# Performance work log

Hardware: AMD Instinct MI355X
Metric: run time of the kernel (lower is better)

Reference implementation:

```python
import jax, jax.numpy as jnp
import numpy as np

B = 16
NUM_CN = 25000
NUM_VN = 50000
NUM_EDGES = 200000
D_EMBED = 16
D_HIDDEN = 32
D_MSG = 16


def setup_inputs() -> dict:
    key = jax.random.key(0)
    ks = jax.random.split(key, 16)
    def w(k, fan_in, fan_out):
        return jax.random.normal(k, (fan_in, fan_out), dtype=jnp.float32) / jnp.sqrt(jnp.float32(fan_in))
    return {
        "h_from_x": jax.random.normal(ks[0], (B, NUM_CN, D_EMBED), dtype=jnp.float32),
        "h_from_z": jax.random.normal(ks[1], (B, NUM_CN, D_EMBED), dtype=jnp.float32),
        "h_to": jax.random.normal(ks[2], (B, NUM_VN, D_EMBED), dtype=jnp.float32),
        "syndrome_x": jax.random.randint(ks[3], (B, NUM_CN), 0, 2, dtype=jnp.int32),
        "syndrome_z": jax.random.randint(ks[4], (B, NUM_CN), 0, 2, dtype=jnp.int32),
        "from_ind_x": jax.random.randint(ks[5], (NUM_EDGES,), 0, NUM_CN, dtype=jnp.int32),
        "to_ind_x": jax.random.randint(ks[6], (NUM_EDGES,), 0, NUM_VN, dtype=jnp.int32),
        "from_ind_z": jax.random.randint(ks[7], (NUM_EDGES,), 0, NUM_CN, dtype=jnp.int32),
        "to_ind_z": jax.random.randint(ks[8], (NUM_EDGES,), 0, NUM_VN, dtype=jnp.int32),
        # msg MLP x: [2*D_EMBED -> D_HIDDEN (relu) -> D_MSG], no bias
        "Wx1": w(ks[9], 2 * D_EMBED, D_HIDDEN),
        "Wx2": w(ks[10], D_HIDDEN, D_MSG),
        "Wz1": w(ks[11], 2 * D_EMBED, D_HIDDEN),
        "Wz2": w(ks[12], D_HIDDEN, D_MSG),
        # embed MLP: [2*D_MSG + D_EMBED -> D_HIDDEN (relu) -> D_EMBED], no bias
        "We1": w(ks[13], 2 * D_MSG + D_EMBED, D_HIDDEN),
        "We2": w(ks[14], D_HIDDEN, D_EMBED),
    }


def _edge_messages(h_from, h_to, syn, from_ind, to_ind, W1, W2):
    # gather edge endpoint embeddings -> [B, E, 2*D_EMBED]
    feat = jnp.concatenate([h_from[:, from_ind, :], h_to[:, to_ind, :]], axis=-1)
    msg = jnp.maximum(feat @ W1, 0.0) @ W2          # [B, E, D_MSG]
    mask = syn[:, from_ind].astype(msg.dtype)[..., None]
    return msg * mask


def _segment_reduce_sum(msg, to_ind, num_vn):
    # ragged gather+sum per receiving vertex == segment_sum over to_ind
    # msg: [B, E, D] -> [E, B, D] -> segment_sum -> [N, B, D] -> [B, N, D]
    m = jax.ops.segment_sum(jnp.transpose(msg, (1, 0, 2)), to_ind, num_segments=num_vn)
    return jnp.transpose(m, (1, 0, 2))


def reference(h_from_x, h_from_z, h_to, syndrome_x, syndrome_z,
              from_ind_x, to_ind_x, from_ind_z, to_ind_z,
              Wx1, Wx2, Wz1, Wz2, We1, We2):
    num_vn = h_to.shape[1]
    msg_x = _edge_messages(h_from_x, h_to, syndrome_x, from_ind_x, to_ind_x, Wx1, Wx2)
    msg_z = _edge_messages(h_from_z, h_to, syndrome_z, from_ind_z, to_ind_z, Wz1, Wz2)
    m_x = _segment_reduce_sum(msg_x, to_ind_x, num_vn)  # [B, N, D_MSG]
    m_z = _segment_reduce_sum(msg_z, to_ind_z, num_vn)
    feat = jnp.concatenate([m_x, m_z, h_to], axis=-1)   # [B, N, 2*D_MSG+D_EMBED]
    h_to_new = jnp.maximum(feat @ We1, 0.0) @ We2
    return h_to_new
```

## Files before the change

kernel.cpp:

```cpp
#include <hip/hip_runtime.h>

#define NUM_CN   25000
#define NUM_VN   50000
#define NUM_E    200000
#define D_EMBED  16
#define D_HIDDEN 32
#define D_MSG    16
#define BATCH    16

#define WS_IDS_X   0
#define WS_IDS_Z   200000
#define WS_OFF_X   400000
#define WS_OFF_Z   450001
#define WS_CNT_X   500002
#define WS_CNT_Z   550002
#define WS_CUR_X   600002
#define WS_CUR_Z   650002
#define WS_INCL_X  700002
#define WS_INCL_Z  751202
#define WS_PSUM    802402
#define WS_BASE    802530
#define WS_A1X     802816
#define WS_A1Z     7202816
#define SCAN_CHUNKS 49

__global__ __launch_bounds__(256) void hist_kernel(
    const int* __restrict__ ti_x, const int* __restrict__ ti_z,
    int* __restrict__ cnt_x, int* __restrict__ cnt_z)
{
    int e = blockIdx.x * 256 + threadIdx.x;
    if (e >= NUM_E) return;
    atomicAdd(&cnt_x[ti_x[e]], 1);
    atomicAdd(&cnt_z[ti_z[e]], 1);
}

__global__ __launch_bounds__(1024) void scan1_kernel(
    const int* __restrict__ cnt_x, const int* __restrict__ cnt_z,
    int* __restrict__ incl_x, int* __restrict__ incl_z,
    int* __restrict__ psum)
{
    __shared__ int s[1024];
    const int ch  = blockIdx.y;
    const int blk = blockIdx.x;
    const int t   = threadIdx.x;
    const int gid = blk * 1024 + t;
    const int* cnt  = ch ? cnt_z  : cnt_x;
    int*       incl = ch ? incl_z : incl_x;
    int v = (gid < NUM_VN) ? cnt[gid] : 0;
    s[t] = v;
    __syncthreads();
#pragma unroll
    for (int d = 1; d < 1024; d <<= 1) {
        int x = 0;
        if (t >= d) x = s[t - d];
        __syncthreads();
        if (t >= d) s[t] += x;
        __syncthreads();
    }
    incl[gid] = s[t];
    if (t == 1023) psum[ch * 64 + blk] = s[1023];
}

__global__ void scan2_kernel(const int* __restrict__ psum, int* __restrict__ base)
{
    int ch = threadIdx.x;
    if (ch >= 2) return;
    int run = 0;
    for (int i = 0; i < SCAN_CHUNKS; ++i) {
        base[ch * 64 + i] = run;
        run += psum[ch * 64 + i];
    }
}

__global__ __launch_bounds__(1024) void scan3_kernel(
    const int* __restrict__ cnt_x, const int* __restrict__ cnt_z,
    const int* __restrict__ incl_x, const int* __restrict__ incl_z,
    const int* __restrict__ base,
    int* __restrict__ off_x, int* __restrict__ off_z,
    int* __restrict__ cur_x, int* __restrict__ cur_z)
{
    const int ch  = blockIdx.y;
    const int blk = blockIdx.x;
    const int t   = threadIdx.x;
    const int i   = blk * 1024 + t;
    if (i >= NUM_VN) return;
    const int* cnt  = ch ? cnt_z  : cnt_x;
    const int* incl = ch ? incl_z : incl_x;
    int*       off  = ch ? off_z  : off_x;
    int*       cur  = ch ? cur_z  : cur_x;
    int bs = base[ch * 64 + blk];
    int iv = incl[i];
    off[i + 1] = bs + iv;
    cur[i]     = bs + iv - cnt[i];
    if (i == 0) off[0] = 0;
}

__global__ __launch_bounds__(256) void fill_kernel(
    const int* __restrict__ ti_x, const int* __restrict__ ti_z,
    const int* __restrict__ fi_x, const int* __restrict__ fi_z,
    int* __restrict__ cur_x, int* __restrict__ cur_z,
    int* __restrict__ ids_x, int* __restrict__ ids_z)
{
    int e = blockIdx.x * 256 + threadIdx.x;
    if (e >= NUM_E) return;
    int px = atomicAdd(&cur_x[ti_x[e]], 1);
    ids_x[px] = fi_x[e];
    int pz = atomicAdd(&cur_z[ti_z[e]], 1);
    ids_z[pz] = fi_z[e];
}

__global__ __launch_bounds__(256) void pack_bits_kernel(
    const int* __restrict__ syn_x, const int* __restrict__ syn_z,
    unsigned* __restrict__ bits_x, unsigned* __restrict__ bits_z)
{
    int cn = blockIdx.x * 256 + threadIdx.x;
    if (cn >= NUM_CN) return;
    unsigned wx = 0, wz = 0;
#pragma unroll
    for (int b = 0; b < BATCH; ++b) {
        wx |= (unsigned)(syn_x[b * NUM_CN + cn] & 1) << b;
        wz |= (unsigned)(syn_z[b * NUM_CN + cn] & 1) << b;
    }
    bits_x[cn] = wx;
    bits_z[cn] = wz;
}

__device__ __forceinline__ unsigned pack_bf16(float a, float b) {
    unsigned ua = __float_as_uint(a); ua += 0x7fff + ((ua >> 16) & 1);
    unsigned ub = __float_as_uint(b); ub += 0x7fff + ((ub >> 16) & 1);
    return (ua >> 16) | (ub & 0xffff0000u);
}

__global__ __launch_bounds__(256) void a1_kernel(
    const float* __restrict__ h_from_x, const float* __restrict__ h_from_z,
    const float* __restrict__ Wx1, const float* __restrict__ Wz1,
    uint4* __restrict__ a1x, uint4* __restrict__ a1z)
{
    int t = blockIdx.x * 256 + threadIdx.x;
    if (t >= NUM_CN * BATCH) return;
    const int ch = blockIdx.y;
    const int b  = t & 15;
    const int cn = t >> 4;
    const float* hsrc = (ch ? h_from_z : h_from_x) + ((size_t)b * NUM_CN + cn) * D_EMBED;
    const float* W1   = ch ? Wz1 : Wx1;
    uint4* dst = (ch ? a1z : a1x) + (size_t)cn * 64;

    float hf[D_EMBED];
#pragma unroll
    for (int i = 0; i < 4; ++i) {
        float4 v = ((const float4*)hsrc)[i];
        hf[4 * i + 0] = v.x; hf[4 * i + 1] = v.y;
        hf[4 * i + 2] = v.z; hf[4 * i + 3] = v.w;
    }
    float a[D_HIDDEN];
#pragma unroll
    for (int j = 0; j < D_HIDDEN; ++j) a[j] = 0.0f;
#pragma unroll
    for (int i = 0; i < D_EMBED; ++i) {
        const float fi = hf[i];
#pragma unroll
        for (int j = 0; j < D_HIDDEN; ++j)
            a[j] = fmaf(fi, W1[i * D_HIDDEN + j], a[j]);
    }
    unsigned u[16];
#pragma unroll
    for (int j = 0; j < 16; ++j) u[j] = pack_bf16(a[2 * j], a[2 * j + 1]);
#pragma unroll
    for (int p = 0; p < 4; ++p) {
        uint4 q;
        q.x = u[4 * p + 0]; q.y = u[4 * p + 1];
        q.z = u[4 * p + 2]; q.w = u[4 * p + 3];
        dst[p * 16 + b] = q;
    }
}

__device__ __forceinline__ void channel_accum(
    const float* __restrict__ h_to_slot, int n, int b,
    const int* __restrict__ off, const int* __restrict__ ids,
    const unsigned* __restrict__ bits,
    const uint4* __restrict__ a1,
    const float* __restrict__ W1, const float* __restrict__ W2,
    unsigned* __restrict__ um)
{
    float ht[D_EMBED];
#pragma unroll
    for (int i = 0; i < 4; ++i) {
        float4 v = ((const float4*)h_to_slot)[i];
        ht[4 * i + 0] = v.x; ht[4 * i + 1] = v.y;
        ht[4 * i + 2] = v.z; ht[4 * i + 3] = v.w;
    }
    float2 a2[16];
#pragma unroll
    for (int p = 0; p < 16; ++p) { a2[p].x = 0.0f; a2[p].y = 0.0f; }
#pragma unroll
    for (int i = 0; i < D_EMBED; ++i) {
        const float hi = ht[i];
        const float* w = W1 + (D_EMBED + i) * D_HIDDEN;
#pragma unroll
        for (int p = 0; p < 16; ++p) {
            a2[p].x = fmaf(hi, w[2 * p],     a2[p].x);
            a2[p].y = fmaf(hi, w[2 * p + 1], a2[p].y);
        }
    }

    float2 hacc[16];
#pragma unroll
    for (int p = 0; p < 16; ++p) { hacc[p].x = 0.0f; hacc[p].y = 0.0f; }

    const int ks = off[n], ke = off[n + 1];
    for (int k = ks; k < ke; ++k) {
        const int from = ids[k];
        const unsigned mw = bits[from];
        const uint4* pa = a1 + (size_t)from * 64 + b;
        uint4 q0 = pa[0], q1 = pa[16], q2 = pa[32], q3 = pa[48];
        const float fm = (float)((mw >> b) & 1u);
        unsigned uu[16] = {q0.x, q0.y, q0.z, q0.w,
                           q1.x, q1.y, q1.z, q1.w,
                           q2.x, q2.y, q2.z, q2.w,
                           q3.x, q3.y, q3.z, q3.w};
#pragma unroll
        for (int p = 0; p < 16; ++p) {
            float lo = __uint_as_float(uu[p] << 16);
            float hi = __uint_as_float(uu[p] & 0xffff0000u);
            hacc[p].x = fmaf(fm, fmaxf(a2[p].x + lo, 0.0f), hacc[p].x);
            hacc[p].y = fmaf(fm, fmaxf(a2[p].y + hi, 0.0f), hacc[p].y);
        }
    }

    float m[D_MSG];
#pragma unroll
    for (int j = 0; j < D_MSG; ++j) m[j] = 0.0f;
#pragma unroll
    for (int p = 0; p < 16; ++p) {
        const float h0 = hacc[p].x, h1 = hacc[p].y;
        const float* w0 = W2 + (2 * p) * D_MSG;
        const float* w1 = W2 + (2 * p + 1) * D_MSG;
#pragma unroll
        for (int j = 0; j < D_MSG; ++j)
            m[j] = fmaf(h0, w0[j], fmaf(h1, w1[j], m[j]));
    }
#pragma unroll
    for (int j = 0; j < 8; ++j) um[j] = pack_bf16(m[2 * j], m[2 * j + 1]);
}

__global__ __launch_bounds__(256) void gather_kernel(
    const float* __restrict__ h_to,
    const unsigned* __restrict__ bits_x, const unsigned* __restrict__ bits_z,
    const int* __restrict__ off_x, const int* __restrict__ ids_x,
    const int* __restrict__ off_z, const int* __restrict__ ids_z,
    const uint4* __restrict__ a1x, const uint4* __restrict__ a1z,
    const float* __restrict__ Wx1, const float* __restrict__ Wx2,
    const float* __restrict__ Wz1, const float* __restrict__ Wz2,
    uint4* __restrict__ out_m)
{
    const int t = blockIdx.x * 256 + threadIdx.x;
    if (t >= NUM_VN * BATCH) return;
    const int b = t & (BATCH - 1);
    const int n = t >> 4;
    const size_t slot = (size_t)b * NUM_VN + n;
    const float* ht_slot = h_to + slot * D_EMBED;

    unsigned um[16];
    channel_accum(ht_slot, n, b, off_x, ids_x, bits_x, a1x, Wx1, Wx2, um);
    channel_accum(ht_slot, n, b, off_z, ids_z, bits_z, a1z, Wz1, Wz2, um + 8);

    uint4* dst = out_m + slot * 4;
#pragma unroll
    for (int p = 0; p < 4; ++p) {
        uint4 q;
        q.x = um[4 * p + 0]; q.y = um[4 * p + 1];
        q.z = um[4 * p + 2]; q.w = um[4 * p + 3];
        dst[p] = q;
    }
}

__global__ __launch_bounds__(256) void node_kernel(
    const float* __restrict__ h_to,
    const float* __restrict__ We1, const float* __restrict__ We2,
    float* out)
{
    const int t = blockIdx.x * 256 + threadIdx.x;
    if (t >= NUM_VN * BATCH) return;
    const int b = t & (BATCH - 1);
    const int n = t >> 4;
    const size_t slot = (size_t)b * NUM_VN + n;

    const uint4* pm = (const uint4*)out + slot * 4;
    uint4 q0 = pm[0], q1 = pm[1], q2 = pm[2], q3 = pm[3];
    unsigned uu[16] = {q0.x, q0.y, q0.z, q0.w,
                       q1.x, q1.y, q1.z, q1.w,
                       q2.x, q2.y, q2.z, q2.w,
                       q3.x, q3.y, q3.z, q3.w};
    float f[48];
#pragma unroll
    for (int p = 0; p < 16; ++p) {
        f[2 * p]     = __uint_as_float(uu[p] << 16);
        f[2 * p + 1] = __uint_as_float(uu[p] & 0xffff0000u);
    }
#pragma unroll
    for (int i = 0; i < 4; ++i) {
        float4 v = ((const float4*)(h_to + slot * D_EMBED))[i];
        f[32 + 4 * i + 0] = v.x; f[32 + 4 * i + 1] = v.y;
        f[32 + 4 * i + 2] = v.z; f[32 + 4 * i + 3] = v.w;
    }

    float2 hid[16];
#pragma unroll
    for (int p = 0; p < 16; ++p) { hid[p].x = 0.0f; hid[p].y = 0.0f; }
#pragma unroll
    for (int i = 0; i < 48; ++i) {
        const float fi = f[i];
        const float* w = We1 + i * D_HIDDEN;
#pragma unroll
        for (int p = 0; p < 16; ++p) {
            hid[p].x = fmaf(fi, w[2 * p],     hid[p].x);
            hid[p].y = fmaf(fi, w[2 * p + 1], hid[p].y);
        }
    }
#pragma unroll
    for (int p = 0; p < 16; ++p) {
        hid[p].x = fmaxf(hid[p].x, 0.0f);
        hid[p].y = fmaxf(hid[p].y, 0.0f);
    }

    float o[D_EMBED];
#pragma unroll
    for (int k = 0; k < D_EMBED; ++k) o[k] = 0.0f;
#pragma unroll
    for (int p = 0; p < 16; ++p) {
        const float h0 = hid[p].x, h1 = hid[p].y;
        const float* w0 = We2 + (2 * p) * D_EMBED;
        const float* w1 = We2 + (2 * p + 1) * D_EMBED;
#pragma unroll
        for (int k = 0; k < D_EMBED; ++k)
            o[k] = fmaf(h0, w0[k], fmaf(h1, w1[k], o[k]));
    }

#pragma unroll
    for (int i = 0; i < 4; ++i) {
        float4 v;
        v.x = o[4 * i + 0]; v.y = o[4 * i + 1];
        v.z = o[4 * i + 2]; v.w = o[4 * i + 3];
        ((float4*)(out + slot * D_EMBED))[i] = v;
    }
}

extern "C" void kernel_launch(void* const* d_in, const int* in_sizes, int n_in,
                              void* d_out, int out_size, void* d_ws, size_t ws_size,
                              hipStream_t stream) {
    const float* h_from_x = (const float*)d_in[0];
    const float* h_from_z = (const float*)d_in[1];
    const float* h_to     = (const float*)d_in[2];
    const int*   syn_x    = (const int*)d_in[3];
    const int*   syn_z    = (const int*)d_in[4];
    const int*   fi_x     = (const int*)d_in[5];
    const int*   ti_x     = (const int*)d_in[6];
    const int*   fi_z     = (const int*)d_in[7];
    const int*   ti_z     = (const int*)d_in[8];
    const float* Wx1      = (const float*)d_in[9];
    const float* Wx2      = (const float*)d_in[10];
    const float* Wz1      = (const float*)d_in[11];
    const float* Wz2      = (const float*)d_in[12];
    const float* We1      = (const float*)d_in[13];
    const float* We2      = (const float*)d_in[14];

    int* ws = (int*)d_ws;
    int* ids_x  = ws + WS_IDS_X;
    int* ids_z  = ws + WS_IDS_Z;
    int* off_x  = ws + WS_OFF_X;
    int* off_z  = ws + WS_OFF_Z;
    int* cnt_x  = ws + WS_CNT_X;
    int* cnt_z  = ws + WS_CNT_Z;
    int* cur_x  = ws + WS_CUR_X;
    int* cur_z  = ws + WS_CUR_Z;
    int* incl_x = ws + WS_INCL_X;
    int* incl_z = ws + WS_INCL_Z;
    int* psum   = ws + WS_PSUM;
    int* base   = ws + WS_BASE;
    uint4* a1x  = (uint4*)(ws + WS_A1X);
    uint4* a1z  = (uint4*)(ws + WS_A1Z);

    unsigned* bits_x = (unsigned*)cur_x;
    unsigned* bits_z = (unsigned*)cur_z;

    hipMemsetAsync(cnt_x, 0, 2 * NUM_VN * sizeof(int), stream);

    hist_kernel<<<dim3((NUM_E + 255) / 256), dim3(256), 0, stream>>>(
        ti_x, ti_z, cnt_x, cnt_z);
    scan1_kernel<<<dim3(SCAN_CHUNKS, 2), dim3(1024), 0, stream>>>(
        cnt_x, cnt_z, incl_x, incl_z, psum);
    scan2_kernel<<<dim3(1), dim3(64), 0, stream>>>(psum, base);
    scan3_kernel<<<dim3(SCAN_CHUNKS, 2), dim3(1024), 0, stream>>>(
        cnt_x, cnt_z, incl_x, incl_z, base, off_x, off_z, cur_x, cur_z);
    fill_kernel<<<dim3((NUM_E + 255) / 256), dim3(256), 0, stream>>>(
        ti_x, ti_z, fi_x, fi_z, cur_x, cur_z, ids_x, ids_z);
    pack_bits_kernel<<<dim3((NUM_CN + 255) / 256), dim3(256), 0, stream>>>(
        syn_x, syn_z, bits_x, bits_z);

    a1_kernel<<<dim3((NUM_CN * BATCH + 255) / 256, 2), dim3(256), 0, stream>>>(
        h_from_x, h_from_z, Wx1, Wz1, a1x, a1z);

    gather_kernel<<<dim3((NUM_VN * BATCH) / 256), dim3(256), 0, stream>>>(
        h_to, bits_x, bits_z, off_x, ids_x, off_z, ids_z, a1x, a1z,
        Wx1, Wx2, Wz1, Wz2, (uint4*)d_out);

    node_kernel<<<dim3((NUM_VN * BATCH) / 256), dim3(256), 0, stream>>>(
        h_to, We1, We2, (float*)d_out);
}
```

Baseline: 416.0 us.

## Fuse gather and node MLP kernels, fold syndrome mask into precomputed activations

Merges the gather and node kernels into one, so per-node messages stay in registers in fp32 instead of making a bf16 round trip through the output buffer. The syndrome mask is folded into a1 by writing bf16 -inf for masked edges, so ReLU yields zero and the per-edge bits lookup and multiply go away. The edge loop is unrolled by two so more independent gather loads are in flight. The cost is higher register pressure from the fused kernel, with launch bounds now requesting 4 blocks per CU, which may cause spills.

```diff
diff --git a/kernel.cpp b/kernel.cpp
--- a/kernel.cpp
+++ b/kernel.cpp
@@ -134,6 +134,7 @@
 __global__ __launch_bounds__(256) void a1_kernel(
     const float* __restrict__ h_from_x, const float* __restrict__ h_from_z,
     const float* __restrict__ Wx1, const float* __restrict__ Wz1,
+    const unsigned* __restrict__ bits_x, const unsigned* __restrict__ bits_z,
     uint4* __restrict__ a1x, uint4* __restrict__ a1z)
 {
     int t = blockIdx.x * 256 + threadIdx.x;
@@ -143,6 +144,8 @@
     const int cn = t >> 4;
     const float* hsrc = (ch ? h_from_z : h_from_x) + ((size_t)b * NUM_CN + cn) * D_EMBED;
     const float* W1   = ch ? Wz1 : Wx1;
+    const unsigned mw = (ch ? bits_z : bits_x)[cn];
+    const bool on = (mw >> b) & 1u;
     uint4* dst = (ch ? a1z : a1x) + (size_t)cn * 64;
 
     float hf[D_EMBED];
@@ -164,7 +167,8 @@
     }
     unsigned u[16];
 #pragma unroll
-    for (int j = 0; j < 16; ++j) u[j] = pack_bf16(a[2 * j], a[2 * j + 1]);
+    for (int j = 0; j < 16; ++j)
+        u[j] = on ? pack_bf16(a[2 * j], a[2 * j + 1]) : 0xFF80FF80u;
 #pragma unroll
     for (int p = 0; p < 4; ++p) {
         uint4 q;
@@ -174,13 +178,29 @@
     }
 }
 
+__device__ __forceinline__ void consume_edge(
+    const uint4 q0, const uint4 q1, const uint4 q2, const uint4 q3,
+    const float2* __restrict__ act, float2* __restrict__ hacc)
+{
+    unsigned uu[16] = {q0.x, q0.y, q0.z, q0.w,
+                       q1.x, q1.y, q1.z, q1.w,
+                       q2.x, q2.y, q2.z, q2.w,
+                       q3.x, q3.y, q3.z, q3.w};
+#pragma unroll
+    for (int p = 0; p < 16; ++p) {
+        float lo = __uint_as_float(uu[p] << 16);
+        float hi = __uint_as_float(uu[p] & 0xffff0000u);
+        hacc[p].x += fmaxf(act[p].x + lo, 0.0f);
+        hacc[p].y += fmaxf(act[p].y + hi, 0.0f);
+    }
+}
+
 __device__ __forceinline__ void channel_accum(
     const float* __restrict__ h_to_slot, int n, int b,
     const int* __restrict__ off, const int* __restrict__ ids,
-    const unsigned* __restrict__ bits,
     const uint4* __restrict__ a1,
     const float* __restrict__ W1, const float* __restrict__ W2,
-    unsigned* __restrict__ um)
+    float* __restrict__ mout)
 {
     float ht[D_EMBED];
 #pragma unroll
@@ -189,17 +209,17 @@
         ht[4 * i + 0] = v.x; ht[4 * i + 1] = v.y;
         ht[4 * i + 2] = v.z; ht[4 * i + 3] = v.w;
     }
-    float2 a2[16];
-#pragma unroll
-    for (int p = 0; p < 16; ++p) { a2[p].x = 0.0f; a2[p].y = 0.0f; }
+    float2 act[16];
+#pragma unroll
+    for (int p = 0; p < 16; ++p) { act[p].x = 0.0f; act[p].y = 0.0f; }
 #pragma unroll
     for (int i = 0; i < D_EMBED; ++i) {
         const float hi = ht[i];
         const float* w = W1 + (D_EMBED + i) * D_HIDDEN;
 #pragma unroll
         for (int p = 0; p < 16; ++p) {
-            a2[p].x = fmaf(hi, w[2 * p],     a2[p].x);
-            a2[p].y = fmaf(hi, w[2 * p + 1], a2[p].y);
+            act[p].x = fmaf(hi, w[2 * p],     act[p].x);
+            act[p].y = fmaf(hi, w[2 * p + 1], act[p].y);
         }
     }
 
@@ -208,23 +228,18 @@
     for (int p = 0; p < 16; ++p) { hacc[p].x = 0.0f; hacc[p].y = 0.0f; }
 
     const int ks = off[n], ke = off[n + 1];
-    for (int k = ks; k < ke; ++k) {
-        const int from = ids[k];
-        const unsigned mw = bits[from];
-        const uint4* pa = a1 + (size_t)from * 64 + b;
-        uint4 q0 = pa[0], q1 = pa[16], q2 = pa[32], q3 = pa[48];
-        const float fm = (float)((mw >> b) & 1u);
-        unsigned uu[16] = {q0.x, q0.y, q0.z, q0.w,
-                           q1.x, q1.y, q1.z, q1.w,
-                           q2.x, q2.y, q2.z, q2.w,
-                           q3.x, q3.y, q3.z, q3.w};
-#pragma unroll
-        for (int p = 0; p < 16; ++p) {
-            float lo = __uint_as_float(uu[p] << 16);
-            float hi = __uint_as_float(uu[p] & 0xffff0000u);
-            hacc[p].x = fmaf(fm, fmaxf(a2[p].x + lo, 0.0f), hacc[p].x);
-            hacc[p].y = fmaf(fm, fmaxf(a2[p].y + hi, 0.0f), hacc[p].y);
-        }
+    int k = ks;
+    for (; k + 1 < ke; k += 2) {
+        const uint4* pa = a1 + (size_t)ids[k]     * 64 + b;
+        const uint4* pb = a1 + (size_t)ids[k + 1] * 64 + b;
+        uint4 qa0 = pa[0], qa1 = pa[16], qa2 = pa[32], qa3 = pa[48];
+        uint4 qb0 = pb[0], qb1 = pb[16], qb2 = pb[32], qb3 = pb[48];
+        consume_edge(qa0, qa1, qa2, qa3, act, hacc);
+        consume_edge(qb0, qb1, qb2, qb3, act, hacc);
+    }
+    if (k < ke) {
+        const uint4* pa = a1 + (size_t)ids[k] * 64 + b;
+        consume_edge(pa[0], pa[16], pa[32], pa[48], act, hacc);
     }
 
     float m[D_MSG];
@@ -240,18 +255,18 @@
             m[j] = fmaf(h0, w0[j], fmaf(h1, w1[j], m[j]));
     }
 #pragma unroll
-    for (int j = 0; j < 8; ++j) um[j] = pack_bf16(m[2 * j], m[2 * j + 1]);
-}
-
-__global__ __launch_bounds__(256) void gather_kernel(
+    for (int j = 0; j < D_MSG; ++j) mout[j] = m[j];
+}
+
+__global__ __launch_bounds__(256, 4) void gather_node_kernel(
     const float* __restrict__ h_to,
-    const unsigned* __restrict__ bits_x, const unsigned* __restrict__ bits_z,
     const int* __restrict__ off_x, const int* __restrict__ ids_x,
     const int* __restrict__ off_z, const int* __restrict__ ids_z,
     const uint4* __restrict__ a1x, const uint4* __restrict__ a1z,
     const float* __restrict__ Wx1, const float* __restrict__ Wx2,
     const float* __restrict__ Wz1, const float* __restrict__ Wz2,
-    uint4* __restrict__ out_m)
+    const float* __restrict__ We1, const float* __restrict__ We2,
+    float* __restrict__ out)
 {
     const int t = blockIdx.x * 256 + threadIdx.x;
     if (t >= NUM_VN * BATCH) return;
@@ -260,56 +275,16 @@
     const size_t slot = (size_t)b * NUM_VN + n;
     const float* ht_slot = h_to + slot * D_EMBED;
 
-    unsigned um[16];
-    channel_accum(ht_slot, n, b, off_x, ids_x, bits_x, a1x, Wx1, Wx2, um);
-    channel_accum(ht_slot, n, b, off_z, ids_z, bits_z, a1z, Wz1, Wz2, um + 8);
-
-    uint4* dst = out_m + slot * 4;
-#pragma unroll
-    for (int p = 0; p < 4; ++p) {
-        uint4 q;
-        q.x = um[4 * p + 0]; q.y = um[4 * p + 1];
-        q.z = um[4 * p + 2]; q.w = um[4 * p + 3];
-        dst[p] = q;
-    }
-}
-
-__global__ __launch_bounds__(256) void node_kernel(
-    const float* __restrict__ h_to,
-    const float* __restrict__ We1, const float* __restrict__ We2,
-    float* out)
-{
-    const int t = blockIdx.x * 256 + threadIdx.x;
-    if (t >= NUM_VN * BATCH) return;
-    const int b = t & (BATCH - 1);
-    const int n = t >> 4;
-    const size_t slot = (size_t)b * NUM_VN + n;
-
-    const uint4* pm = (const uint4*)out + slot * 4;
-    uint4 q0 = pm[0], q1 = pm[1], q2 = pm[2], q3 = pm[3];
-    unsigned uu[16] = {q0.x, q0.y, q0.z, q0.w,
-                       q1.x, q1.y, q1.z, q1.w,
-                       q2.x, q2.y, q2.z, q2.w,
-                       q3.x, q3.y, q3.z, q3.w};
-    float f[48];
-#pragma unroll
-    for (int p = 0; p < 16; ++p) {
-        f[2 * p]     = __uint_as_float(uu[p] << 16);
-        f[2 * p + 1] = __uint_as_float(uu[p] & 0xffff0000u);
-    }
-#pragma unroll
-    for (int i = 0; i < 4; ++i) {
-        float4 v = ((const float4*)(h_to + slot * D_EMBED))[i];
-        f[32 + 4 * i + 0] = v.x; f[32 + 4 * i + 1] = v.y;
-        f[32 + 4 * i + 2] = v.z; f[32 + 4 * i + 3] = v.w;
-    }
+    float mall[2 * D_MSG];
+    channel_accum(ht_slot, n, b, off_x, ids_x, a1x, Wx1, Wx2, mall);
+    channel_accum(ht_slot, n, b, off_z, ids_z, a1z, Wz1, Wz2, mall + D_MSG);
 
     float2 hid[16];
 #pragma unroll
     for (int p = 0; p < 16; ++p) { hid[p].x = 0.0f; hid[p].y = 0.0f; }
 #pragma unroll
-    for (int i = 0; i < 48; ++i) {
-        const float fi = f[i];
+    for (int i = 0; i < 2 * D_MSG; ++i) {
+        const float fi = mall[i];
         const float* w = We1 + i * D_HIDDEN;
 #pragma unroll
         for (int p = 0; p < 16; ++p) {
@@ -318,6 +293,21 @@
         }
     }
 #pragma unroll
+    for (int i4 = 0; i4 < 4; ++i4) {
+        float4 v = ((const float4*)ht_slot)[i4];
+        float hv[4] = {v.x, v.y, v.z, v.w};
+#pragma unroll
+        for (int j = 0; j < 4; ++j) {
+            const float fi = hv[j];
+            const float* w = We1 + (2 * D_MSG + 4 * i4 + j) * D_HIDDEN;
+#pragma unroll
+            for (int p = 0; p < 16; ++p) {
+                hid[p].x = fmaf(fi, w[2 * p],     hid[p].x);
+                hid[p].y = fmaf(fi, w[2 * p + 1], hid[p].y);
+            }
+        }
+    }
+#pragma unroll
     for (int p = 0; p < 16; ++p) {
         hid[p].x = fmaxf(hid[p].x, 0.0f);
         hid[p].y = fmaxf(hid[p].y, 0.0f);
@@ -325,15 +315,15 @@
 
     float o[D_EMBED];
 #pragma unroll
-    for (int k = 0; k < D_EMBED; ++k) o[k] = 0.0f;
+    for (int kk = 0; kk < D_EMBED; ++kk) o[kk] = 0.0f;
 #pragma unroll
     for (int p = 0; p < 16; ++p) {
         const float h0 = hid[p].x, h1 = hid[p].y;
         const float* w0 = We2 + (2 * p) * D_EMBED;
         const float* w1 = We2 + (2 * p + 1) * D_EMBED;
 #pragma unroll
-        for (int k = 0; k < D_EMBED; ++k)
-            o[k] = fmaf(h0, w0[k], fmaf(h1, w1[k], o[k]));
+        for (int kk = 0; kk < D_EMBED; ++kk)
+            o[kk] = fmaf(h0, w0[kk], fmaf(h1, w1[kk], o[kk]));
     }
 
 #pragma unroll
@@ -398,12 +388,9 @@
         syn_x, syn_z, bits_x, bits_z);
 
     a1_kernel<<<dim3((NUM_CN * BATCH + 255) / 256, 2), dim3(256), 0, stream>>>(
-        h_from_x, h_from_z, Wx1, Wz1, a1x, a1z);
-
-    gather_kernel<<<dim3((NUM_VN * BATCH) / 256), dim3(256), 0, stream>>>(
-        h_to, bits_x, bits_z, off_x, ids_x, off_z, ids_z, a1x, a1z,
-        Wx1, Wx2, Wz1, Wz2, (uint4*)d_out);
-
-    node_kernel<<<dim3((NUM_VN * BATCH) / 256), dim3(256), 0, stream>>>(
-        h_to, We1, We2, (float*)d_out);
-}
+        h_from_x, h_from_z, Wx1, Wz1, bits_x, bits_z, a1x, a1z);
+
+    gather_node_kernel<<<dim3((NUM_VN * BATCH) / 256), dim3(256), 0, stream>>>(
+        h_to, off_x, ids_x, off_z, ids_z, a1x, a1z,
+        Wx1, Wx2, Wz1, Wz2, We1, We2, (float*)d_out);
+}
```

Measured after the change: 471.6 us. +13.4%, slower.

## Fold syndrome mask into precomputed activations and merge CSR build kernels

Applied to the files above, without the earlier changes.

Masked edges are encoded by writing -inf bf16 values into the per-CN first-layer activations, so relu yields zero and the gather loop no longer loads syndrome bits per edge. The edge loop is unrolled by two to overlap the two random loads. The three-kernel scan becomes a single block-per-channel strip scan, and syndrome bit packing is merged into the histogram kernel, which removes several launches. The single-block scan serializes work onto two blocks, and the -inf trick relies on act plus -inf staying -inf.

```diff
diff --git a/kernel.cpp b/kernel.cpp
--- a/kernel.cpp
+++ b/kernel.cpp
@@ -16,83 +16,75 @@
 #define WS_CNT_Z   550002
 #define WS_CUR_X   600002
 #define WS_CUR_Z   650002
-#define WS_INCL_X  700002
-#define WS_INCL_Z  751202
-#define WS_PSUM    802402
-#define WS_BASE    802530
+#define WS_BITS_X  700002
+#define WS_BITS_Z  751202
 #define WS_A1X     802816
 #define WS_A1Z     7202816
-#define SCAN_CHUNKS 49
-
-__global__ __launch_bounds__(256) void hist_kernel(
+#define SCAN_STRIP 49
+
+__global__ __launch_bounds__(256) void hist_pack_kernel(
     const int* __restrict__ ti_x, const int* __restrict__ ti_z,
-    int* __restrict__ cnt_x, int* __restrict__ cnt_z)
+    const int* __restrict__ syn_x, const int* __restrict__ syn_z,
+    int* __restrict__ cnt_x, int* __restrict__ cnt_z,
+    unsigned* __restrict__ bits_x, unsigned* __restrict__ bits_z)
 {
     int e = blockIdx.x * 256 + threadIdx.x;
-    if (e >= NUM_E) return;
-    atomicAdd(&cnt_x[ti_x[e]], 1);
-    atomicAdd(&cnt_z[ti_z[e]], 1);
-}
-
-__global__ __launch_bounds__(1024) void scan1_kernel(
+    if (e < NUM_E) {
+        atomicAdd(&cnt_x[ti_x[e]], 1);
+        atomicAdd(&cnt_z[ti_z[e]], 1);
+    }
+    if (e < NUM_CN) {
+        unsigned wx = 0, wz = 0;
+#pragma unroll
+        for (int b = 0; b < BATCH; ++b) {
+            wx |= (unsigned)(syn_x[b * NUM_CN + e] & 1) << b;
+            wz |= (unsigned)(syn_z[b * NUM_CN + e] & 1) << b;
+        }
+        bits_x[e] = wx;
+        bits_z[e] = wz;
+    }
+}
+
+__global__ __launch_bounds__(1024) void scan_kernel(
     const int* __restrict__ cnt_x, const int* __restrict__ cnt_z,
-    int* __restrict__ incl_x, int* __restrict__ incl_z,
-    int* __restrict__ psum)
-{
-    __shared__ int s[1024];
-    const int ch  = blockIdx.y;
-    const int blk = blockIdx.x;
-    const int t   = threadIdx.x;
-    const int gid = blk * 1024 + t;
-    const int* cnt  = ch ? cnt_z  : cnt_x;
-    int*       incl = ch ? incl_z : incl_x;
-    int v = (gid < NUM_VN) ? cnt[gid] : 0;
-    s[t] = v;
+    int* __restrict__ off_x, int* __restrict__ off_z,
+    int* __restrict__ cur_x, int* __restrict__ cur_z)
+{
+    const int ch = blockIdx.x;
+    const int* cnt = ch ? cnt_z : cnt_x;
+    int* off = ch ? off_z : off_x;
+    int* cur = ch ? cur_z : cur_x;
+    const int t  = threadIdx.x;
+    const int i0 = t * SCAN_STRIP;
+
+    int s = 0;
+#pragma unroll 7
+    for (int j = 0; j < SCAN_STRIP; ++j) {
+        int i = i0 + j;
+        if (i < NUM_VN) s += cnt[i];
+    }
+    __shared__ int sm[1024];
+    sm[t] = s;
     __syncthreads();
-#pragma unroll
     for (int d = 1; d < 1024; d <<= 1) {
         int x = 0;
-        if (t >= d) x = s[t - d];
+        if (t >= d) x = sm[t - d];
         __syncthreads();
-        if (t >= d) s[t] += x;
+        if (t >= d) sm[t] += x;
         __syncthreads();
     }
-    incl[gid] = s[t];
-    if (t == 1023) psum[ch * 64 + blk] = s[1023];
-}
-
-__global__ void scan2_kernel(const int* __restrict__ psum, int* __restrict__ base)
-{
-    int ch = threadIdx.x;
-    if (ch >= 2) return;
-    int run = 0;
-    for (int i = 0; i < SCAN_CHUNKS; ++i) {
-        base[ch * 64 + i] = run;
-        run += psum[ch * 64 + i];
-    }
-}
-
-__global__ __launch_bounds__(1024) void scan3_kernel(
-    const int* __restrict__ cnt_x, const int* __restrict__ cnt_z,
-    const int* __restrict__ incl_x, const int* __restrict__ incl_z,
-    const int* __restrict__ base,
-    int* __restrict__ off_x, int* __restrict__ off_z,
-    int* __restrict__ cur_x, int* __restrict__ cur_z)
-{
-    const int ch  = blockIdx.y;
-    const int blk = blockIdx.x;
-    const int t   = threadIdx.x;
-    const int i   = blk * 1024 + t;
-    if (i >= NUM_VN) return;
-    const int* cnt  = ch ? cnt_z  : cnt_x;
-    const int* incl = ch ? incl_z : incl_x;
-    int*       off  = ch ? off_z  : off_x;
-    int*       cur  = ch ? cur_z  : cur_x;
-    int bs = base[ch * 64 + blk];
-    int iv = incl[i];
-    off[i + 1] = bs + iv;
-    cur[i]     = bs + iv - cnt[i];
-    if (i == 0) off[0] = 0;
+    int run = (t == 0) ? 0 : sm[t - 1];
+#pragma unroll 7
+    for (int j = 0; j < SCAN_STRIP; ++j) {
+        int i = i0 + j;
+        if (i < NUM_VN) {
+            int c = cnt[i];
+            run += c;
+            off[i + 1] = run;
+            cur[i]     = run - c;
+        }
+    }
+    if (t == 0) off[0] = 0;
 }
 
 __global__ __launch_bounds__(256) void fill_kernel(
@@ -109,22 +101,6 @@
     ids_z[pz] = fi_z[e];
 }
 
-__global__ __launch_bounds__(256) void pack_bits_kernel(
-    const int* __restrict__ syn_x, const int* __restrict__ syn_z,
-    unsigned* __restrict__ bits_x, unsigned* __restrict__ bits_z)
-{
-    int cn = blockIdx.x * 256 + threadIdx.x;
-    if (cn >= NUM_CN) return;
-    unsigned wx = 0, wz = 0;
-#pragma unroll
-    for (int b = 0; b < BATCH; ++b) {
-        wx |= (unsigned)(syn_x[b * NUM_CN + cn] & 1) << b;
-        wz |= (unsigned)(syn_z[b * NUM_CN + cn] & 1) << b;
-    }
-    bits_x[cn] = wx;
-    bits_z[cn] = wz;
-}
-
 __device__ __forceinline__ unsigned pack_bf16(float a, float b) {
     unsigned ua = __float_as_uint(a); ua += 0x7fff + ((ua >> 16) & 1);
     unsigned ub = __float_as_uint(b); ub += 0x7fff + ((ub >> 16) & 1);
@@ -134,6 +110,7 @@
 __global__ __launch_bounds__(256) void a1_kernel(
     const float* __restrict__ h_from_x, const float* __restrict__ h_from_z,
     const float* __restrict__ Wx1, const float* __restrict__ Wz1,
+    const unsigned* __restrict__ bits_x, const unsigned* __restrict__ bits_z,
     uint4* __restrict__ a1x, uint4* __restrict__ a1z)
 {
     int t = blockIdx.x * 256 + threadIdx.x;
@@ -143,6 +120,8 @@
     const int cn = t >> 4;
     const float* hsrc = (ch ? h_from_z : h_from_x) + ((size_t)b * NUM_CN + cn) * D_EMBED;
     const float* W1   = ch ? Wz1 : Wx1;
+    const unsigned mw = (ch ? bits_z : bits_x)[cn];
+    const bool on = (mw >> b) & 1u;
     uint4* dst = (ch ? a1z : a1x) + (size_t)cn * 64;
 
     float hf[D_EMBED];
@@ -164,7 +143,8 @@
     }
     unsigned u[16];
 #pragma unroll
-    for (int j = 0; j < 16; ++j) u[j] = pack_bf16(a[2 * j], a[2 * j + 1]);
+    for (int j = 0; j < 16; ++j)
+        u[j] = on ? pack_bf16(a[2 * j], a[2 * j + 1]) : 0xFF80FF80u;
 #pragma unroll
     for (int p = 0; p < 4; ++p) {
         uint4 q;
@@ -177,7 +157,6 @@
 __device__ __forceinline__ void channel_accum(
     const float* __restrict__ h_to_slot, int n, int b,
     const int* __restrict__ off, const int* __restrict__ ids,
-    const unsigned* __restrict__ bits,
     const uint4* __restrict__ a1,
     const float* __restrict__ W1, const float* __restrict__ W2,
     unsigned* __restrict__ um)
@@ -189,17 +168,17 @@
         ht[4 * i + 0] = v.x; ht[4 * i + 1] = v.y;
         ht[4 * i + 2] = v.z; ht[4 * i + 3] = v.w;
     }
-    float2 a2[16];
-#pragma unroll
-    for (int p = 0; p < 16; ++p) { a2[p].x = 0.0f; a2[p].y = 0.0f; }
+    float2 act[16];
+#pragma unroll
+    for (int p = 0; p < 16; ++p) { act[p].x = 0.0f; act[p].y = 0.0f; }
 #pragma unroll
     for (int i = 0; i < D_EMBED; ++i) {
         const float hi = ht[i];
         const float* w = W1 + (D_EMBED + i) * D_HIDDEN;
 #pragma unroll
         for (int p = 0; p < 16; ++p) {
-            a2[p].x = fmaf(hi, w[2 * p],     a2[p].x);
-            a2[p].y = fmaf(hi, w[2 * p + 1], a2[p].y);
+            act[p].x = fmaf(hi, w[2 * p],     act[p].x);
+            act[p].y = fmaf(hi, w[2 * p + 1], act[p].y);
         }
     }
 
@@ -208,12 +187,38 @@
     for (int p = 0; p < 16; ++p) { hacc[p].x = 0.0f; hacc[p].y = 0.0f; }
 
     const int ks = off[n], ke = off[n + 1];
-    for (int k = ks; k < ke; ++k) {
-        const int from = ids[k];
-        const unsigned mw = bits[from];
-        const uint4* pa = a1 + (size_t)from * 64 + b;
+    int k = ks;
+    for (; k + 1 < ke; k += 2) {
+        const uint4* pa = a1 + (size_t)ids[k]     * 64 + b;
+        const uint4* pb = a1 + (size_t)ids[k + 1] * 64 + b;
+        uint4 qa0 = pa[0], qa1 = pa[16], qa2 = pa[32], qa3 = pa[48];
+        uint4 qb0 = pb[0], qb1 = pb[16], qb2 = pb[32], qb3 = pb[48];
+        unsigned ua[16] = {qa0.x, qa0.y, qa0.z, qa0.w,
+                           qa1.x, qa1.y, qa1.z, qa1.w,
+                           qa2.x, qa2.y, qa2.z, qa2.w,
+                           qa3.x, qa3.y, qa3.z, qa3.w};
+#pragma unroll
+        for (int p = 0; p < 16; ++p) {
+            float lo = __uint_as_float(ua[p] << 16);
+            float hi = __uint_as_float(ua[p] & 0xffff0000u);
+            hacc[p].x += fmaxf(act[p].x + lo, 0.0f);
+            hacc[p].y += fmaxf(act[p].y + hi, 0.0f);
+        }
+        unsigned ub[16] = {qb0.x, qb0.y, qb0.z, qb0.w,
+                           qb1.x, qb1.y, qb1.z, qb1.w,
+                           qb2.x, qb2.y, qb2.z, qb2.w,
+                           qb3.x, qb3.y, qb3.z, qb3.w};
+#pragma unroll
+        for (int p = 0; p < 16; ++p) {
+            float lo = __uint_as_float(ub[p] << 16);
+            float hi = __uint_as_float(ub[p] & 0xffff0000u);
+            hacc[p].x += fmaxf(act[p].x + lo, 0.0f);
+            hacc[p].y += fmaxf(act[p].y + hi, 0.0f);
+        }
+    }
+    if (k < ke) {
+        const uint4* pa = a1 + (size_t)ids[k] * 64 + b;
         uint4 q0 = pa[0], q1 = pa[16], q2 = pa[32], q3 = pa[48];
-        const float fm = (float)((mw >> b) & 1u);
         unsigned uu[16] = {q0.x, q0.y, q0.z, q0.w,
                            q1.x, q1.y, q1.z, q1.w,
                            q2.x, q2.y, q2.z, q2.w,
@@ -222,8 +227,8 @@
         for (int p = 0; p < 16; ++p) {
             float lo = __uint_as_float(uu[p] << 16);
             float hi = __uint_as_float(uu[p] & 0xffff0000u);
-            hacc[p].x = fmaf(fm, fmaxf(a2[p].x + lo, 0.0f), hacc[p].x);
-            hacc[p].y = fmaf(fm, fmaxf(a2[p].y + hi, 0.0f), hacc[p].y);
+            hacc[p].x += fmaxf(act[p].x + lo, 0.0f);
+            hacc[p].y += fmaxf(act[p].y + hi, 0.0f);
         }
     }
 
@@ -245,7 +250,6 @@
 
 __global__ __launch_bounds__(256) void gather_kernel(
     const float* __restrict__ h_to,
-    const unsigned* __restrict__ bits_x, const unsigned* __restrict__ bits_z,
     const int* __restrict__ off_x, const int* __restrict__ ids_x,
     const int* __restrict__ off_z, const int* __restrict__ ids_z,
     const uint4* __restrict__ a1x, const uint4* __restrict__ a1z,
@@ -261,8 +265,8 @@
     const float* ht_slot = h_to + slot * D_EMBED;
 
     unsigned um[16];
-    channel_accum(ht_slot, n, b, off_x, ids_x, bits_x, a1x, Wx1, Wx2, um);
-    channel_accum(ht_slot, n, b, off_z, ids_z, bits_z, a1z, Wz1, Wz2, um + 8);
+    channel_accum(ht_slot, n, b, off_x, ids_x, a1x, Wx1, Wx2, um);
+    channel_accum(ht_slot, n, b, off_z, ids_z, a1z, Wz1, Wz2, um + 8);
 
     uint4* dst = out_m + slot * 4;
 #pragma unroll
@@ -373,35 +377,25 @@
     int* cnt_z  = ws + WS_CNT_Z;
     int* cur_x  = ws + WS_CUR_X;
     int* cur_z  = ws + WS_CUR_Z;
-    int* incl_x = ws + WS_INCL_X;
-    int* incl_z = ws + WS_INCL_Z;
-    int* psum   = ws + WS_PSUM;
-    int* base   = ws + WS_BASE;
+    unsigned* bits_x = (unsigned*)(ws + WS_BITS_X);
+    unsigned* bits_z = (unsigned*)(ws + WS_BITS_Z);
     uint4* a1x  = (uint4*)(ws + WS_A1X);
     uint4* a1z  = (uint4*)(ws + WS_A1Z);
 
-    unsigned* bits_x = (unsigned*)cur_x;
-    unsigned* bits_z = (unsigned*)cur_z;
-
     hipMemsetAsync(cnt_x, 0, 2 * NUM_VN * sizeof(int), stream);
 
-    hist_kernel<<<dim3((NUM_E + 255) / 256), dim3(256), 0, stream>>>(
-        ti_x, ti_z, cnt_x, cnt_z);
-    scan1_kernel<<<dim3(SCAN_CHUNKS, 2), dim3(1024), 0, stream>>>(
-        cnt_x, cnt_z, incl_x, incl_z, psum);
-    scan2_kernel<<<dim3(1), dim3(64), 0, stream>>>(psum, base);
-    scan3_kernel<<<dim3(SCAN_CHUNKS, 2), dim3(1024), 0, stream>>>(
-        cnt_x, cnt_z, incl_x, incl_z, base, off_x, off_z, cur_x, cur_z);
+    hist_pack_kernel<<<dim3((NUM_E + 255) / 256), dim3(256), 0, stream>>>(
+        ti_x, ti_z, syn_x, syn_z, cnt_x, cnt_z, bits_x, bits_z);
+    scan_kernel<<<dim3(2), dim3(1024), 0, stream>>>(
+        cnt_x, cnt_z, off_x, off_z, cur_x, cur_z);
     fill_kernel<<<dim3((NUM_E + 255) / 256), dim3(256), 0, stream>>>(
         ti_x, ti_z, fi_x, fi_z, cur_x, cur_z, ids_x, ids_z);
-    pack_bits_kernel<<<dim3((NUM_CN + 255) / 256), dim3(256), 0, stream>>>(
-        syn_x, syn_z, bits_x, bits_z);
 
     a1_kernel<<<dim3((NUM_CN * BATCH + 255) / 256, 2), dim3(256), 0, stream>>>(
-        h_from_x, h_from_z, Wx1, Wz1, a1x, a1z);
+        h_from_x, h_from_z, Wx1, Wz1, bits_x, bits_z, a1x, a1z);
 
     gather_kernel<<<dim3((NUM_VN * BATCH) / 256), dim3(256), 0, stream>>>(
-        h_to, bits_x, bits_z, off_x, ids_x, off_z, ids_z, a1x, a1z,
+        h_to, off_x, ids_x, off_z, ids_z, a1x, a1z,
         Wx1, Wx2, Wz1, Wz2, (uint4*)d_out);
 
     node_kernel<<<dim3((NUM_VN * BATCH) / 256), dim3(256), 0, stream>>>(
```

After: 600.1 us. +44.3%, slower.

## Split hidden dim across two lanes and fold syndrome mask into precomputed activations

Applied to the files above, without the earlier changes.

The gather kernel now uses two threads per (vertex, batch) slot. Each thread handles half of the 32 hidden units, and the partial message outputs are combined with a cross-lane shuffle. The syndrome mask moves into a1_kernel, which writes bf16 negative infinity for masked source nodes so the ReLU zeroes them. This removes the per-edge bits load and mask multiply. The goal is higher parallelism and occupancy, with fewer registers per thread and a launch bound of 8. The cost is duplicated h_to loads and per-edge index loads across the two half-threads.

```diff
diff --git a/kernel.cpp b/kernel.cpp
--- a/kernel.cpp
+++ b/kernel.cpp
@@ -134,6 +134,7 @@
 __global__ __launch_bounds__(256) void a1_kernel(
     const float* __restrict__ h_from_x, const float* __restrict__ h_from_z,
     const float* __restrict__ Wx1, const float* __restrict__ Wz1,
+    const unsigned* __restrict__ bits_x, const unsigned* __restrict__ bits_z,
     uint4* __restrict__ a1x, uint4* __restrict__ a1z)
 {
     int t = blockIdx.x * 256 + threadIdx.x;
@@ -143,6 +144,8 @@
     const int cn = t >> 4;
     const float* hsrc = (ch ? h_from_z : h_from_x) + ((size_t)b * NUM_CN + cn) * D_EMBED;
     const float* W1   = ch ? Wz1 : Wx1;
+    const unsigned mw = (ch ? bits_z : bits_x)[cn];
+    const bool on = (mw >> b) & 1u;
     uint4* dst = (ch ? a1z : a1x) + (size_t)cn * 64;
 
     float hf[D_EMBED];
@@ -164,7 +167,8 @@
     }
     unsigned u[16];
 #pragma unroll
-    for (int j = 0; j < 16; ++j) u[j] = pack_bf16(a[2 * j], a[2 * j + 1]);
+    for (int j = 0; j < 16; ++j)
+        u[j] = on ? pack_bf16(a[2 * j], a[2 * j + 1]) : 0xFF80FF80u;
 #pragma unroll
     for (int p = 0; p < 4; ++p) {
         uint4 q;
@@ -174,78 +178,69 @@
     }
 }
 
-__device__ __forceinline__ void channel_accum(
-    const float* __restrict__ h_to_slot, int n, int b,
+__device__ __forceinline__ void channel_half(
+    const float* __restrict__ ht_slot, int n, int h, int b,
     const int* __restrict__ off, const int* __restrict__ ids,
-    const unsigned* __restrict__ bits,
     const uint4* __restrict__ a1,
     const float* __restrict__ W1, const float* __restrict__ W2,
-    unsigned* __restrict__ um)
-{
-    float ht[D_EMBED];
-#pragma unroll
-    for (int i = 0; i < 4; ++i) {
-        float4 v = ((const float4*)h_to_slot)[i];
-        ht[4 * i + 0] = v.x; ht[4 * i + 1] = v.y;
-        ht[4 * i + 2] = v.z; ht[4 * i + 3] = v.w;
-    }
-    float2 a2[16];
-#pragma unroll
-    for (int p = 0; p < 16; ++p) { a2[p].x = 0.0f; a2[p].y = 0.0f; }
-#pragma unroll
-    for (int i = 0; i < D_EMBED; ++i) {
-        const float hi = ht[i];
-        const float* w = W1 + (D_EMBED + i) * D_HIDDEN;
-#pragma unroll
-        for (int p = 0; p < 16; ++p) {
-            a2[p].x = fmaf(hi, w[2 * p],     a2[p].x);
-            a2[p].y = fmaf(hi, w[2 * p + 1], a2[p].y);
+    float* __restrict__ m)
+{
+    float2 act[8];
+#pragma unroll
+    for (int p = 0; p < 8; ++p) { act[p].x = 0.0f; act[p].y = 0.0f; }
+#pragma unroll
+    for (int i4 = 0; i4 < 4; ++i4) {
+        float4 v = ((const float4*)ht_slot)[i4];
+        float hv[4] = {v.x, v.y, v.z, v.w};
+#pragma unroll
+        for (int j = 0; j < 4; ++j) {
+            const float fi = hv[j];
+            const float* w = W1 + (D_EMBED + 4 * i4 + j) * D_HIDDEN + 16 * h;
+#pragma unroll
+            for (int p = 0; p < 8; ++p) {
+                act[p].x = fmaf(fi, w[2 * p],     act[p].x);
+                act[p].y = fmaf(fi, w[2 * p + 1], act[p].y);
+            }
         }
     }
 
-    float2 hacc[16];
-#pragma unroll
-    for (int p = 0; p < 16; ++p) { hacc[p].x = 0.0f; hacc[p].y = 0.0f; }
-
+    float2 hacc[8];
+#pragma unroll
+    for (int p = 0; p < 8; ++p) { hacc[p].x = 0.0f; hacc[p].y = 0.0f; }
+
+    const uint4* aL = a1 + h * 32 + b;
     const int ks = off[n], ke = off[n + 1];
     for (int k = ks; k < ke; ++k) {
-        const int from = ids[k];
-        const unsigned mw = bits[from];
-        const uint4* pa = a1 + (size_t)from * 64 + b;
-        uint4 q0 = pa[0], q1 = pa[16], q2 = pa[32], q3 = pa[48];
-        const float fm = (float)((mw >> b) & 1u);
-        unsigned uu[16] = {q0.x, q0.y, q0.z, q0.w,
-                           q1.x, q1.y, q1.z, q1.w,
-                           q2.x, q2.y, q2.z, q2.w,
-                           q3.x, q3.y, q3.z, q3.w};
-#pragma unroll
-        for (int p = 0; p < 16; ++p) {
+        const uint4* pa = aL + (size_t)ids[k] * 64;
+        uint4 q0 = pa[0], q1 = pa[16];
+        unsigned uu[8] = {q0.x, q0.y, q0.z, q0.w,
+                          q1.x, q1.y, q1.z, q1.w};
+#pragma unroll
+        for (int p = 0; p < 8; ++p) {
             float lo = __uint_as_float(uu[p] << 16);
             float hi = __uint_as_float(uu[p] & 0xffff0000u);
-            hacc[p].x = fmaf(fm, fmaxf(a2[p].x + lo, 0.0f), hacc[p].x);
-            hacc[p].y = fmaf(fm, fmaxf(a2[p].y + hi, 0.0f), hacc[p].y);
+            hacc[p].x += fmaxf(act[p].x + lo, 0.0f);
+            hacc[p].y += fmaxf(act[p].y + hi, 0.0f);
         }
     }
 
-    float m[D_MSG];
 #pragma unroll
     for (int j = 0; j < D_MSG; ++j) m[j] = 0.0f;
 #pragma unroll
-    for (int p = 0; p < 16; ++p) {
+    for (int p = 0; p < 8; ++p) {
+        const float* w0 = W2 + (16 * h + 2 * p) * D_MSG;
+        const float* w1 = w0 + D_MSG;
         const float h0 = hacc[p].x, h1 = hacc[p].y;
-        const float* w0 = W2 + (2 * p) * D_MSG;
-        const float* w1 = W2 + (2 * p + 1) * D_MSG;
 #pragma unroll
         for (int j = 0; j < D_MSG; ++j)
             m[j] = fmaf(h0, w0[j], fmaf(h1, w1[j], m[j]));
     }
 #pragma unroll
-    for (int j = 0; j < 8; ++j) um[j] = pack_bf16(m[2 * j], m[2 * j + 1]);
-}
-
-__global__ __launch_bounds__(256) void gather_kernel(
+    for (int j = 0; j < D_MSG; ++j) m[j] += __shfl_xor(m[j], 16, 64);
+}
+
+__global__ __launch_bounds__(256, 8) void gather_kernel(
     const float* __restrict__ h_to,
-    const unsigned* __restrict__ bits_x, const unsigned* __restrict__ bits_z,
     const int* __restrict__ off_x, const int* __restrict__ ids_x,
     const int* __restrict__ off_z, const int* __restrict__ ids_z,
     const uint4* __restrict__ a1x, const uint4* __restrict__ a1z,
@@ -254,23 +249,35 @@
     uint4* __restrict__ out_m)
 {
     const int t = blockIdx.x * 256 + threadIdx.x;
-    if (t >= NUM_VN * BATCH) return;
-    const int b = t & (BATCH - 1);
-    const int n = t >> 4;
+    const int b = t & 15;
+    const int h = (t >> 4) & 1;
+    const int n = t >> 5;
     const size_t slot = (size_t)b * NUM_VN + n;
     const float* ht_slot = h_to + slot * D_EMBED;
-
-    unsigned um[16];
-    channel_accum(ht_slot, n, b, off_x, ids_x, bits_x, a1x, Wx1, Wx2, um);
-    channel_accum(ht_slot, n, b, off_z, ids_z, bits_z, a1z, Wz1, Wz2, um + 8);
-
     uint4* dst = out_m + slot * 4;
-#pragma unroll
-    for (int p = 0; p < 4; ++p) {
+
+    float m[D_MSG];
+
+    channel_half(ht_slot, n, h, b, off_x, ids_x, a1x, Wx1, Wx2, m);
+    if (h == 0) {
         uint4 q;
-        q.x = um[4 * p + 0]; q.y = um[4 * p + 1];
-        q.z = um[4 * p + 2]; q.w = um[4 * p + 3];
-        dst[p] = q;
+        q.x = pack_bf16(m[0], m[1]); q.y = pack_bf16(m[2], m[3]);
+        q.z = pack_bf16(m[4], m[5]); q.w = pack_bf16(m[6], m[7]);
+        dst[0] = q;
+        q.x = pack_bf16(m[8],  m[9]);  q.y = pack_bf16(m[10], m[11]);
+        q.z = pack_bf16(m[12], m[13]); q.w = pack_bf16(m[14], m[15]);
+        dst[1] = q;
+    }
+
+    channel_half(ht_slot, n, h, b, off_z, ids_z, a1z, Wz1, Wz2, m);
+    if (h == 1) {
+        uint4 q;
+        q.x = pack_bf16(m[0], m[1]); q.y = pack_bf16(m[2], m[3]);
+        q.z = pack_bf16(m[4], m[5]); q.w = pack_bf16(m[6], m[7]);
+        dst[2] = q;
+        q.x = pack_bf16(m[8],  m[9]);  q.y = pack_bf16(m[10], m[11]);
+        q.z = pack_bf16(m[12], m[13]); q.w = pack_bf16(m[14], m[15]);
+        dst[3] = q;
     }
 }
 
@@ -398,10 +405,10 @@
         syn_x, syn_z, bits_x, bits_z);
 
     a1_kernel<<<dim3((NUM_CN * BATCH + 255) / 256, 2), dim3(256), 0, stream>>>(
-        h_from_x, h_from_z, Wx1, Wz1, a1x, a1z);
-
-    gather_kernel<<<dim3((NUM_VN * BATCH) / 256), dim3(256), 0, stream>>>(
-        h_to, bits_x, bits_z, off_x, ids_x, off_z, ids_z, a1x, a1z,
+        h_from_x, h_from_z, Wx1, Wz1, bits_x, bits_z, a1x, a1z);
+
+    gather_kernel<<<dim3((NUM_VN * 2 * BATCH) / 256), dim3(256), 0, stream>>>(
+        h_to, off_x, ids_x, off_z, ids_z, a1x, a1z,
         Wx1, Wx2, Wz1, Wz2, (uint4*)d_out);
 
     node_kernel<<<dim3((NUM_VN * BATCH) / 256), dim3(256), 0, stream>>>(
```

Result: slower. 824.0 us (+98.1%).
